# Performance work log

Hardware: AMD Instinct MI355X
Metric: run time of the kernel (lower is better)

## Reference

```python
import jax, jax.numpy as jnp
import numpy as np

NMS_THRESH = 0.5
SCORE_THRESH = 0.05
MAX_DET = 300


def _iou_one_vs_all(box, boxes):
    # box: [4] (x1,y1,x2,y2); boxes: [N,4]
    x1 = jnp.maximum(box[0], boxes[:, 0])
    y1 = jnp.maximum(box[1], boxes[:, 1])
    x2 = jnp.minimum(box[2], boxes[:, 2])
    y2 = jnp.minimum(box[3], boxes[:, 3])
    inter = jnp.maximum(x2 - x1, 0.0) * jnp.maximum(y2 - y1, 0.0)
    area_a = (box[2] - box[0]) * (box[3] - box[1])
    area_b = (boxes[:, 2] - boxes[:, 0]) * (boxes[:, 3] - boxes[:, 1])
    union = area_a + area_b - inter
    return inter / jnp.maximum(union, 1e-8)


def _nms_single_class(boxes, scores):
    # Greedy NMS with max_output_size=MAX_DET, matching tf.image.non_max_suppression
    # after score-threshold prefiltering. boxes:[N,4], scores:[N].
    s0 = jnp.where(scores > SCORE_THRESH, scores, -jnp.inf)

    def step(s, _):
        i = jnp.argmax(s)
        si = s[i]
        sel = jnp.isfinite(si)  # False once no candidates remain
        iou = _iou_one_vs_all(boxes[i], boxes)
        s = jnp.where(sel & (iou > NMS_THRESH), -jnp.inf, s)
        s = s.at[i].set(-jnp.inf)
        return s, (i, si, sel)

    _, (idx, sv, sel) = jax.lax.scan(step, s0, None, length=MAX_DET)
    # unselected slots carry -inf score
    return idx.astype(jnp.int32), jnp.where(sel, sv, -jnp.inf)


def _filter_one_image(boxes, classification, other):
    # boxes:[N,4], classification:[N,C], other:[N,D]
    C = classification.shape[1]
    # class-specific NMS (class_specific_filter=True, nms=True)
    idx, sv = jax.vmap(lambda c: _nms_single_class(boxes, classification[:, c]))(
        jnp.arange(C))  # each [C, MAX_DET]
    labels = jnp.broadcast_to(jnp.arange(C)[:, None], idx.shape)
    cand_scores = sv.reshape(-1)          # [C*MAX_DET]
    cand_idx = idx.reshape(-1)
    cand_lab = labels.reshape(-1)
    # global top-k over all per-class survivors
    top_s, top_i = jax.lax.top_k(cand_scores, MAX_DET)
    sel_idx = cand_idx[top_i]
    sel_lab = cand_lab[top_i]
    valid = jnp.isfinite(top_s)
    # pad invalid slots with -1 (matches tf.pad(..., constant_values=-1))
    out_boxes = jnp.where(valid[:, None], boxes[sel_idx], -1.0)
    out_scores = jnp.where(valid, top_s, -1.0)
    out_labels = jnp.where(valid, sel_lab, -1).astype(jnp.int32)
    out_other = jnp.where(valid[:, None], other[sel_idx], -1.0)
    return out_boxes, out_scores, out_labels, out_other


def setup_inputs() -> dict:
    key = jax.random.key(0)
    k1, k2, k3, k4 = jax.random.split(key, 4)
    B, N, C, D = 16, 50000, 8, 2
    xy = jax.random.uniform(k1, (B, N, 2), jnp.float32, 0.0, 512.0)
    wh = jax.random.uniform(k2, (B, N, 2), jnp.float32, 4.0, 100.0)
    boxes = jnp.concatenate([xy, xy + wh], axis=-1)  # valid (x1,y1,x2,y2)
    classification = jax.random.uniform(k3, (B, N, C), jnp.float32)
    other = jax.random.normal(k4, (B, N, D), jnp.float32)
    return {"boxes": boxes, "classification": classification, "other": other}


def reference(boxes, classification, other):
    # tf.map_fn over batch -> vmap over batch
    return jax.vmap(_filter_one_image)(boxes, classification, other)
```

## Files before the change

kernel.cpp:

```cpp
#include <hip/hip_runtime.h>
#include <math.h>
#include <stdint.h>

#define NB 16
#define NN 50000
#define NC 8
#define ND 2
#define MAX_DET 300
#define NMS_T 0.5f
#define SCORE_T 0.05f
#define CAP 1024
#define CUTBIN 252
#define LBUF 128
#define NTILE32 32
#define CHUNK 256
#define NT 1024
#define NPI (NN * NC)
#define F4PB (NPI / 4 / NTILE32)

typedef unsigned long long u64;

__device__ __forceinline__ float neg_inf() { return -__builtin_inff(); }

__device__ __forceinline__ bool iou_gt(float ax1, float ay1, float ax2, float ay2,
                                       float area_a,
                                       float bx1, float by1, float bx2, float by2,
                                       float area_b) {
    float x1 = fmaxf(ax1, bx1), y1 = fmaxf(ay1, by1);
    float x2 = fminf(ax2, bx2), y2 = fminf(ay2, by2);
    float inter = __fmul_rn(fmaxf(__fsub_rn(x2, x1), 0.0f),
                            fmaxf(__fsub_rn(y2, y1), 0.0f));
    float uni = __fsub_rn(__fadd_rn(area_a, area_b), inter);
    return inter > __fmul_rn(0.5f, fmaxf(uni, 1e-8f));
}

__device__ __forceinline__ u64 score_key(float s, int n) {
    unsigned u = __float_as_uint(s);
    u ^= (u & 0x80000000u) ? 0xFFFFFFFFu : 0x80000000u;
    return ((u64)u << 32) | (unsigned)(~(unsigned)n);
}

__device__ __forceinline__ u64 shfl_xor_u64(u64 v, int m) {
    unsigned lo = (unsigned)v, hi = (unsigned)(v >> 32);
    lo = __shfl_xor(lo, m, 64);
    hi = __shfl_xor(hi, m, 64);
    return ((u64)hi << 32) | lo;
}

__global__ __launch_bounds__(1024) void compact_kernel(
    const float* __restrict__ cls, int* __restrict__ tcnt_g,
    u64* __restrict__ cand)
{
    const int b = blockIdx.x >> 5, t32 = blockIdx.x & 31;
    const int tid = threadIdx.x;
    __shared__ u64 buf[8][LBUF];
    __shared__ int lcnt[8];
    if (tid < 8) lcnt[tid] = 0;
    __syncthreads();

    const float4* c4 = (const float4*)(cls + (size_t)b * NPI);
    const int f0 = t32 * F4PB, fend = f0 + F4PB;

    for (int f = f0 + tid; f < fend; f += 1024) {
        float4 v = c4[f];
        int cb = (f & 1) * 4;
        int n = f >> 1;
        float vv[4] = {v.x, v.y, v.z, v.w};
        #pragma unroll
        for (int k = 0; k < 4; ++k) {
            float s = vv[k];
            if (s > SCORE_T) {
                int bn = (int)(s * 256.0f); if (bn > 255) bn = 255;
                if (bn >= CUTBIN) {
                    int c = cb + k;
                    int pos = atomicAdd(&lcnt[c], 1);
                    if (pos < LBUF) buf[c][pos] = score_key(s, n);
                }
            }
        }
    }
    __syncthreads();
    {
        int c = tid >> 7, i = tid & (LBUF - 1);
        int m = lcnt[c];
        if (i < (m < LBUF ? m : LBUF))
            cand[(size_t)(((b * 8 + c) * NTILE32) + t32) * LBUF + i] = buf[c][i];
        if (i == 0) tcnt_g[(b * 8 + c) * NTILE32 + t32] = m;
    }
}

__global__ __launch_bounds__(NT) void nms_fused(
    const float* __restrict__ boxes, const float* __restrict__ cls,
    const u64* __restrict__ cand, const int* __restrict__ tcnt_g,
    int* __restrict__ sel_idx, float* __restrict__ sel_score)
{
    const int bc = blockIdx.x;
    const int b = bc >> 3, c = bc & 7;
    const int tid = threadIdx.x;
    const int lane = tid & 63;
    const float4* bx4 = (const float4*)(boxes + (size_t)b * NN * 4);
    const float* sr = cls + (size_t)b * NN * NC + c;
    int* si = sel_idx + bc * MAX_DET;
    float* ss = sel_score + bc * MAX_DET;

    __shared__ u64 keys[CAP];
    __shared__ int tcnt_s[NTILE32], toff_s[NTILE32];
    __shared__ int sh_total, sh_ovf;
    __shared__ u64 M64[4][CHUNK];
    __shared__ unsigned presup4[4][CHUNK];
    __shared__ float4 cbox2[2][CHUNK];
    __shared__ float  carea2[2][CHUNK];
    __shared__ int    cidx2[2][CHUNK];
    __shared__ float  cscore2[2][CHUNK];
    __shared__ u64 accs4_s[4];
    __shared__ float4 abox[MAX_DET];
    __shared__ float aarea[MAX_DET];
    __shared__ unsigned bm[(NN + 31) / 32];
    __shared__ float rv[NT];
    __shared__ int   ri[NT];
    __shared__ float sboxsh[5];

    if (tid < 64) {
        int v = (lane < NTILE32) ? tcnt_g[bc * NTILE32 + lane] : 0;
        int incl = v;
        #pragma unroll
        for (int d = 1; d < 32; d <<= 1) {
            int o = __shfl_up(incl, d, 64);
            if (lane >= d) incl += o;
        }
        if (lane < NTILE32) { tcnt_s[lane] = v; toff_s[lane] = incl - v; }
        u64 ov = __ballot(lane < NTILE32 && v > LBUF);
        if (lane == 31) { sh_total = incl; sh_ovf = (ov != 0); }
    }
    __syncthreads();
    const int cnt = sh_total;
    const bool full_fb = sh_ovf || (cnt > CAP);
    const int inSet = cnt < CAP ? cnt : CAP;

    int n_acc = 0;
    if (!full_fb) {
        for (int i = tid; i < CAP; i += NT) keys[i] = 0ull;
        __syncthreads();
        for (int s = tid; s < NTILE32 * LBUF; s += NT) {
            int t = s >> 7, i = s & (LBUF - 1);
            if (i < tcnt_s[t])
                keys[toff_s[t] + i] = cand[(size_t)(bc * NTILE32 + t) * LBUF + i];
        }
        __syncthreads();

        const int p0 = (tid >> 6) * 128 + lane, p1 = p0 + 64;
        u64 v0 = 0, v1 = 0;
        if (tid < 512) {
            v0 = keys[p0]; v1 = keys[p1];
            #pragma unroll
            for (int k = 2; k <= 128; k <<= 1) {
                #pragma unroll
                for (int j = k >> 1; j > 0; j >>= 1) {
                    if (j == 64) {
                        bool dir = ((p0 & k) == 0);
                        if ((v0 < v1) == dir) { u64 t = v0; v0 = v1; v1 = t; }
                    } else {
                        bool lower = ((lane & j) == 0);
                        bool dir0 = ((p0 & k) == 0);
                        bool dir1 = ((p1 & k) == 0);
                        u64 o0 = shfl_xor_u64(v0, j);
                        u64 mx0 = v0 > o0 ? v0 : o0, mn0 = v0 > o0 ? o0 : v0;
                        v0 = (lower == dir0) ? mx0 : mn0;
                        u64 o1 = shfl_xor_u64(v1, j);
                        u64 mx1 = v1 > o1 ? v1 : o1, mn1 = v1 > o1 ? o1 : v1;
                        v1 = (lower == dir1) ? mx1 : mn1;
                    }
                }
            }
        }
        __syncthreads();
        for (int k = 256; k <= CAP; k <<= 1) {
            if (tid < 512) { keys[p0] = v0; keys[p1] = v1; }
            __syncthreads();
            for (int j = k >> 1; j >= 128; j >>= 1) {
                if (tid < 512) {
                    int p = tid;
                    int i = 2 * p - (p & (j - 1));
                    int ix = i + j;
                    bool dir = ((i & k) == 0);
                    u64 a = keys[i], b2 = keys[ix];
                    if ((a < b2) == dir) { keys[i] = b2; keys[ix] = a; }
                }
                __syncthreads();
            }
            if (tid < 512) {
                v0 = keys[p0]; v1 = keys[p1];
                {
                    bool dir = ((p0 & k) == 0);
                    if ((v0 < v1) == dir) { u64 t = v0; v0 = v1; v1 = t; }
                }
                #pragma unroll
                for (int j = 32; j > 0; j >>= 1) {
                    bool lower = ((lane & j) == 0);
                    bool dir = ((p0 & k) == 0);
                    u64 o0 = shfl_xor_u64(v0, j);
                    u64 mx0 = v0 > o0 ? v0 : o0, mn0 = v0 > o0 ? o0 : v0;
                    v0 = (lower == dir) ? mx0 : mn0;
                    u64 o1 = shfl_xor_u64(v1, j);
                    u64 mx1 = v1 > o1 ? v1 : o1, mn1 = v1 > o1 ? o1 : v1;
                    v1 = (lower == dir) ? mx1 : mn1;
                }
            }
            __syncthreads();
        }
        if (tid < 512) { keys[p0] = v0; keys[p1] = v1; }
        __syncthreads();

        if (tid < CHUNK && tid < inSet) {
            u64 key = keys[tid];
            int idx = (int)(~(unsigned)key);
            unsigned u = (unsigned)(key >> 32);
            unsigned uo = (u & 0x80000000u) ? (u ^ 0x80000000u) : (~u);
            float4 bb = bx4[idx];
            cbox2[0][tid] = bb;
            carea2[0][tid] = __fmul_rn(__fsub_rn(bb.z, bb.x), __fsub_rn(bb.w, bb.y));
            cidx2[0][tid] = idx; cscore2[0][tid] = __uint_as_float(uo);
        }
        __syncthreads();

        int base = 0, cur = 0;
        while (n_acc < MAX_DET && base < inSet) {
            int m = inSet - base; if (m > CHUNK) m = CHUNK;

            {
                int i = tid & (CHUNK - 1);
                int q = tid >> 8;
                if (i < m) {
                    float4 B = cbox2[cur][i];
                    float  Barea = carea2[cur][i];
                    unsigned p = 0;
                    int t = q;
                    for (; t + 28 < n_acc; t += 32) {
                        float4 A0 = abox[t];      float r0 = aarea[t];
                        float4 A1 = abox[t + 4];  float r1 = aarea[t + 4];
                        float4 A2 = abox[t + 8];  float r2 = aarea[t + 8];
                        float4 A3 = abox[t + 12]; float r3 = aarea[t + 12];
                        float4 A4 = abox[t + 16]; float r4 = aarea[t + 16];
                        float4 A5 = abox[t + 20]; float r5 = aarea[t + 20];
                        float4 A6 = abox[t + 24]; float r6 = aarea[t + 24];
                        float4 A7 = abox[t + 28]; float r7 = aarea[t + 28];
                        bool s0 = iou_gt(A0.x,A0.y,A0.z,A0.w,r0,B.x,B.y,B.z,B.w,Barea);
                        bool s1 = iou_gt(A1.x,A1.y,A1.z,A1.w,r1,B.x,B.y,B.z,B.w,Barea);
                        bool s2 = iou_gt(A2.x,A2.y,A2.z,A2.w,r2,B.x,B.y,B.z,B.w,Barea);
                        bool s3 = iou_gt(A3.x,A3.y,A3.z,A3.w,r3,B.x,B.y,B.z,B.w,Barea);
                        bool s4 = iou_gt(A4.x,A4.y,A4.z,A4.w,r4,B.x,B.y,B.z,B.w,Barea);
                        bool s5 = iou_gt(A5.x,A5.y,A5.z,A5.w,r5,B.x,B.y,B.z,B.w,Barea);
                        bool s6 = iou_gt(A6.x,A6.y,A6.z,A6.w,r6,B.x,B.y,B.z,B.w,Barea);
                        bool s7 = iou_gt(A7.x,A7.y,A7.z,A7.w,r7,B.x,B.y,B.z,B.w,Barea);
                        if (s0|s1|s2|s3|s4|s5|s6|s7) { p = 1; break; }
                    }
                    if (!p) {
                        for (; t < n_acc; t += 4) {
                            float4 A = abox[t];
                            if (iou_gt(A.x,A.y,A.z,A.w,aarea[t],
                                       B.x,B.y,B.z,B.w,Barea)) { p = 1; break; }
                        }
                    }
                    presup4[q][i] = p;
                    u64 bits = 0;
                    int j0 = q * 64;
                    int jend = i - j0; if (jend > 64) jend = 64; if (jend < 0) jend = 0;
                    int jj = 0;
                    for (; jj + 7 < jend; jj += 8) {
                        int j = j0 + jj;
                        float4 A0 = cbox2[cur][j];     float r0 = carea2[cur][j];
                        float4 A1 = cbox2[cur][j + 1]; float r1 = carea2[cur][j + 1];
                        float4 A2 = cbox2[cur][j + 2]; float r2 = carea2[cur][j + 2];
                        float4 A3 = cbox2[cur][j + 3]; float r3 = carea2[cur][j + 3];
                        float4 A4 = cbox2[cur][j + 4]; float r4 = carea2[cur][j + 4];
                        float4 A5 = cbox2[cur][j + 5]; float r5 = carea2[cur][j + 5];
                        float4 A6 = cbox2[cur][j + 6]; float r6 = carea2[cur][j + 6];
                        float4 A7 = cbox2[cur][j + 7]; float r7 = carea2[cur][j + 7];
                        if (iou_gt(A0.x,A0.y,A0.z,A0.w,r0,B.x,B.y,B.z,B.w,Barea)) bits |= 1ull << jj;
                        if (iou_gt(A1.x,A1.y,A1.z,A1.w,r1,B.x,B.y,B.z,B.w,Barea)) bits |= 1ull << (jj+1);
                        if (iou_gt(A2.x,A2.y,A2.z,A2.w,r2,B.x,B.y,B.z,B.w,Barea)) bits |= 1ull << (jj+2);
                        if (iou_gt(A3.x,A3.y,A3.z,A3.w,r3,B.x,B.y,B.z,B.w,Barea)) bits |= 1ull << (jj+3);
                        if (iou_gt(A4.x,A4.y,A4.z,A4.w,r4,B.x,B.y,B.z,B.w,Barea)) bits |= 1ull << (jj+4);
                        if (iou_gt(A5.x,A5.y,A5.z,A5.w,r5,B.x,B.y,B.z,B.w,Barea)) bits |= 1ull << (jj+5);
                        if (iou_gt(A6.x,A6.y,A6.z,A6.w,r6,B.x,B.y,B.z,B.w,Barea)) bits |= 1ull << (jj+6);
                        if (iou_gt(A7.x,A7.y,A7.z,A7.w,r7,B.x,B.y,B.z,B.w,Barea)) bits |= 1ull << (jj+7);
                    }
                    for (; jj < jend; ++jj) {
                        int j = j0 + jj;
                        float4 A = cbox2[cur][j];
                        if (iou_gt(A.x,A.y,A.z,A.w,carea2[cur][j],
                                   B.x,B.y,B.z,B.w,Barea)) bits |= 1ull << jj;
                    }
                    M64[q][i] = bits;
                }
            }
            __syncthreads();

            int nbase = base + m;
            if (tid < 64) {
                u64 Mr[4][4];
                unsigned pe[4];
                bool acc[4];
                #pragma unroll
                for (int cg = 0; cg < 4; ++cg) {
                    int i = cg * 64 + lane;
                    if (i < m) {
                        pe[cg] = presup4[0][i] | presup4[1][i] | presup4[2][i] | presup4[3][i];
                        #pragma unroll
                        for (int w = 0; w < 4; ++w) Mr[cg][w] = M64[w][i];
                    } else {
                        pe[cg] = 1u;
                        #pragma unroll
                        for (int w = 0; w < 4; ++w) Mr[cg][w] = 0ull;
                    }
                    acc[cg] = (pe[cg] == 0);
                }
                u64 a0 = __ballot(acc[0]), a1 = __ballot(acc[1]);
                u64 a2 = __ballot(acc[2]), a3 = __ballot(acc[3]);
                for (int it = 0; it < CHUNK + 1; ++it) {
                    #pragma unroll
                    for (int cg = 0; cg < 4; ++cg) {
                        u64 sup = (Mr[cg][0] & a0) | (Mr[cg][1] & a1)
                                | (Mr[cg][2] & a2) | (Mr[cg][3] & a3);
                        acc[cg] = (pe[cg] == 0) && (sup == 0ull);
                    }
                    u64 n0 = __ballot(acc[0]), n1 = __ballot(acc[1]);
                    u64 n2 = __ballot(acc[2]), n3 = __ballot(acc[3]);
                    bool same = (n0 == a0) && (n1 == a1) && (n2 == a2) && (n3 == a3);
                    a0 = n0; a1 = n1; a2 = n2; a3 = n3;
                    if (same) break;
                }
                if (lane == 0) { accs4_s[0] = a0; accs4_s[1] = a1;
                                 accs4_s[2] = a2; accs4_s[3] = a3; }
            } else if (tid >= 256 && tid < 512 && nbase < inSet) {
                int w = tid - 256;
                if (nbase + w < inSet) {
                    u64 key = keys[nbase + w];
                    int idx = (int)(~(unsigned)key);
                    unsigned u = (unsigned)(key >> 32);
                    unsigned uo = (u & 0x80000000u) ? (u ^ 0x80000000u) : (~u);
                    float4 bb = bx4[idx];
                    cbox2[cur ^ 1][w] = bb;
                    carea2[cur ^ 1][w] = __fmul_rn(__fsub_rn(bb.z, bb.x), __fsub_rn(bb.w, bb.y));
                    cidx2[cur ^ 1][w] = idx; cscore2[cur ^ 1][w] = __uint_as_float(uo);
                }
            }
            __syncthreads();

            u64 a0 = accs4_s[0], a1 = accs4_s[1], a2 = accs4_s[2], a3 = accs4_s[3];
            int add = __popcll(a0) + __popcll(a1) + __popcll(a2) + __popcll(a3);
            if (tid < m) {
                int gg = tid >> 6, o = tid & 63;
                u64 aw = (gg == 0) ? a0 : (gg == 1) ? a1 : (gg == 2) ? a2 : a3;
                if ((aw >> o) & 1ull) {
                    int rank = 0;
                    if (gg > 0) rank += __popcll(a0);
                    if (gg > 1) rank += __popcll(a1);
                    if (gg > 2) rank += __popcll(a2);
                    rank += __popcll(aw & ((1ull << o) - 1ull));
                    int pos = n_acc + rank;
                    if (pos < MAX_DET) {
                        abox[pos] = cbox2[cur][tid]; aarea[pos] = carea2[cur][tid];
                        si[pos] = cidx2[cur][tid]; ss[pos] = cscore2[cur][tid];
                    }
                }
            }
            n_acc += add; if (n_acc > MAX_DET) n_acc = MAX_DET;
            base = nbase; cur ^= 1;
            __syncthreads();
        }
    }

    const bool part_fb = (!full_fb) && (n_acc < MAX_DET);

    if (full_fb || part_fb) {
        const int BMW = (NN + 31) / 32;
        for (int i = tid; i < BMW; i += NT) bm[i] = 0u;
        __syncthreads();
        if (full_fb) {
            n_acc = 0;
        } else {
            for (int n = tid; n < NN; n += NT) {
                float4 bbn = bx4[n];
                float nb_area = __fmul_rn(__fsub_rn(bbn.z, bbn.x), __fsub_rn(bbn.w, bbn.y));
                int s = 0;
                for (int t = 0; t < n_acc; ++t) {
                    float4 A = abox[t];
                    if (iou_gt(A.x, A.y, A.z, A.w, aarea[t],
                               bbn.x, bbn.y, bbn.z, bbn.w, nb_area)) s = 1;
                }
                if (s) atomicOr(&bm[n >> 5], 1u << (n & 31));
            }
        }
        __syncthreads();

        for (int k = n_acc; k < MAX_DET; ++k) {
            float bv = neg_inf(); int bi = 0x7fffffff;
            for (int n = tid; n < NN; n += NT) {
                if (!((bm[n >> 5] >> (n & 31)) & 1u)) {
                    float v = sr[(size_t)n * NC];
                    if (v > SCORE_T && v > bv) { bv = v; bi = n; }
                }
            }
            rv[tid] = bv; ri[tid] = bi;
            __syncthreads();
            for (int s = NT / 2; s > 0; s >>= 1) {
                if (tid < s) {
                    float ov = rv[tid + s]; int oi = ri[tid + s];
                    if (ov > rv[tid] || (ov == rv[tid] && oi < ri[tid])) { rv[tid] = ov; ri[tid] = oi; }
                }
                __syncthreads();
            }
            float mval = rv[0]; int midx = ri[0];
            if (mval == neg_inf()) {
                for (int kk = k + tid; kk < MAX_DET; kk += NT) { si[kk] = 0; ss[kk] = neg_inf(); }
                break;
            }
            if (tid == 0) {
                si[k] = midx; ss[k] = mval;
                float4 sb = bx4[midx];
                sboxsh[0] = sb.x; sboxsh[1] = sb.y; sboxsh[2] = sb.z; sboxsh[3] = sb.w;
                sboxsh[4] = __fmul_rn(__fsub_rn(sb.z, sb.x), __fsub_rn(sb.w, sb.y));
            }
            __syncthreads();
            float ax1 = sboxsh[0], ay1 = sboxsh[1], ax2 = sboxsh[2], ay2 = sboxsh[3];
            float area_a = sboxsh[4];
            for (int n = tid; n < NN; n += NT) {
                float4 bbn = bx4[n];
                float nb_area = __fmul_rn(__fsub_rn(bbn.z, bbn.x), __fsub_rn(bbn.w, bbn.y));
                if (iou_gt(ax1, ay1, ax2, ay2, area_a,
                           bbn.x, bbn.y, bbn.z, bbn.w, nb_area))
                    atomicOr(&bm[n >> 5], 1u << (n & 31));
            }
            __syncthreads();
        }
    } else {
        for (int kk = n_acc + tid; kk < MAX_DET; kk += NT) { si[kk] = 0; ss[kk] = neg_inf(); }
    }
}

__global__ __launch_bounds__(1024) void topk_kernel(
    const float* __restrict__ boxes, const float* __restrict__ other,
    const int* __restrict__ sel_idx, const float* __restrict__ sel_score,
    float* __restrict__ out)
{
    const int b = blockIdx.x;
    const int tid = threadIdx.x;
    const int NCAND = NC * MAX_DET;
    __shared__ u64 lists[NC][MAX_DET];

    for (int i = tid; i < NCAND; i += 1024) {
        float v = sel_score[b * NCAND + i];
        unsigned u = __float_as_uint(v);
        u ^= (u & 0x80000000u) ? 0xFFFFFFFFu : 0x80000000u;
        lists[i / MAX_DET][i % MAX_DET] = ((u64)u << 32) | (unsigned)(~(unsigned)i);
    }
    __syncthreads();

    const float4* bx4 = (const float4*)(boxes + (size_t)b * NN * 4);
    const float*  ot  = other + (size_t)b * NN * ND;
    float* ob = out;
    float* os = out + NB * MAX_DET * 4;
    float* ol = os + NB * MAX_DET;
    float* oo = ol + NB * MAX_DET;

    for (int i = tid; i < NCAND; i += 1024) {
        int cown = i / MAX_DET, slot = i - cown * MAX_DET;
        u64 K = lists[cown][slot];
        int rank = slot;
        int pos[NC], len[NC];
        #pragma unroll
        for (int c2 = 0; c2 < NC; ++c2) {
            pos[c2] = 0;
            len[c2] = (c2 == cown) ? 0 : MAX_DET;
        }
        for (int step = 0; step < 10; ++step) {
            #pragma unroll
            for (int c2 = 0; c2 < NC; ++c2) {
                if (len[c2] > 0) {
                    int half = len[c2] >> 1;
                    bool go = lists[c2][pos[c2] + half] > K;
                    pos[c2] = go ? pos[c2] + half + 1 : pos[c2];
                    len[c2] = go ? len[c2] - half - 1 : half;
                }
            }
        }
        #pragma unroll
        for (int c2 = 0; c2 < NC; ++c2) rank += pos[c2];

        if (rank < MAX_DET) {
            unsigned u = (unsigned)(K >> 32);
            unsigned uo = (u & 0x80000000u) ? (u ^ 0x80000000u) : (u ^ 0xFFFFFFFFu);
            float score = __uint_as_float(uo);
            bool valid = isfinite(score);
            float b0=-1.f,b1=-1.f,b2=-1.f,b3=-1.f,scv=-1.f,lab=-1.f,o0=-1.f,o1=-1.f;
            if (valid) {
                int n = sel_idx[b * NCAND + i];
                float4 bb = bx4[n];
                b0 = bb.x; b1 = bb.y; b2 = bb.z; b3 = bb.w;
                scv = score; lab = (float)cown;
                o0 = ot[n * ND + 0]; o1 = ot[n * ND + 1];
            }
            int base = b * MAX_DET + rank;
            ob[base * 4 + 0] = b0; ob[base * 4 + 1] = b1;
            ob[base * 4 + 2] = b2; ob[base * 4 + 3] = b3;
            os[base] = scv; ol[base] = lab;
            oo[base * 2 + 0] = o0; oo[base * 2 + 1] = o1;
        }
    }
}

extern "C" void kernel_launch(void* const* d_in, const int* in_sizes, int n_in,
                              void* d_out, int out_size, void* d_ws, size_t ws_size,
                              hipStream_t stream) {
    const float* boxes = (const float*)d_in[0];
    const float* cls   = (const float*)d_in[1];
    const float* other = (const float*)d_in[2];
    float* out = (float*)d_out;

    int* tcnt_g = (int*)d_ws;
    u64* cand  = (u64*)(tcnt_g + NB * NC * NTILE32);
    int* sel_idx = (int*)(cand + (size_t)NB * NC * NTILE32 * LBUF);
    float* sel_score = (float*)(sel_idx + NB * NC * MAX_DET);

    compact_kernel<<<NB * NTILE32, 1024, 0, stream>>>(cls, tcnt_g, cand);
    nms_fused<<<NB * NC, NT, 0, stream>>>(boxes, cls, cand, tcnt_g,
                                          sel_idx, sel_score);
    topk_kernel<<<NB, 1024, 0, stream>>>(boxes, other, sel_idx, sel_score, out);
}
```

Baseline: 66.06 us.

## Split fused NMS into sort, global IoU-matrix, and resolve kernels

Replaces the single fused per-class NMS kernel with three kernels. One sorts the candidates, one builds a 512x512 suppression bitmask matrix in global memory using four times as many small blocks, and one resolves greedy acceptance with a single-wavefront fixed-point iteration. The goal is to spread the quadratic IoU work over more CUs instead of 128 large blocks processed chunk by chunk. The costs are two extra launches and global round-trips for keys and the matrix. The stage is also capped at 512 sorted candidates, so more results depend on the slow full-scan fallback when fewer than 300 are accepted.

```diff
diff --git a/kernel.cpp b/kernel.cpp
--- a/kernel.cpp
+++ b/kernel.cpp
@@ -13,8 +13,7 @@
 #define CUTBIN 252
 #define LBUF 128
 #define NTILE32 32
-#define CHUNK 256
-#define NT 1024
+#define STG 512
 #define NPI (NN * NC)
 #define F4PB (NPI / 4 / NTILE32)
 
@@ -89,9 +88,168 @@
     }
 }
 
-__global__ __launch_bounds__(NT) void nms_fused(
+__global__ __launch_bounds__(512) void sort_kernel(
+    const u64* __restrict__ cand, const int* __restrict__ tcnt_g,
+    u64* __restrict__ skeys, int* __restrict__ meta)
+{
+    const int bc = blockIdx.x;
+    const int tid = threadIdx.x;
+    const int lane = tid & 63;
+    __shared__ u64 keys[CAP];
+    __shared__ int tcnt_s[NTILE32], toff_s[NTILE32];
+    __shared__ int sh_total, sh_ovf;
+
+    if (tid < 64) {
+        int v = (lane < NTILE32) ? tcnt_g[bc * NTILE32 + lane] : 0;
+        int incl = v;
+        #pragma unroll
+        for (int d = 1; d < 32; d <<= 1) {
+            int o = __shfl_up(incl, d, 64);
+            if (lane >= d) incl += o;
+        }
+        if (lane < NTILE32) { tcnt_s[lane] = v; toff_s[lane] = incl - v; }
+        u64 ov = __ballot(lane < NTILE32 && v > LBUF);
+        if (lane == 31) { sh_total = incl; sh_ovf = (ov != 0); }
+    }
+    __syncthreads();
+    const int cnt = sh_total;
+    const bool full_fb = sh_ovf || (cnt > CAP);
+    if (full_fb) {
+        if (tid == 0) meta[bc] = -1;
+        return;
+    }
+    if (tid == 0) meta[bc] = cnt;
+
+    for (int i = tid; i < CAP; i += 512) keys[i] = 0ull;
+    __syncthreads();
+    for (int s = tid; s < NTILE32 * LBUF; s += 512) {
+        int t = s >> 7, i = s & (LBUF - 1);
+        if (i < tcnt_s[t])
+            keys[toff_s[t] + i] = cand[(size_t)(bc * NTILE32 + t) * LBUF + i];
+    }
+    __syncthreads();
+
+    const int p0 = (tid >> 6) * 128 + lane, p1 = p0 + 64;
+    u64 v0 = keys[p0], v1 = keys[p1];
+    #pragma unroll
+    for (int k = 2; k <= 128; k <<= 1) {
+        #pragma unroll
+        for (int j = k >> 1; j > 0; j >>= 1) {
+            if (j == 64) {
+                bool dir = ((p0 & k) == 0);
+                if ((v0 < v1) == dir) { u64 t = v0; v0 = v1; v1 = t; }
+            } else {
+                bool lower = ((lane & j) == 0);
+                bool dir0 = ((p0 & k) == 0);
+                bool dir1 = ((p1 & k) == 0);
+                u64 o0 = shfl_xor_u64(v0, j);
+                u64 mx0 = v0 > o0 ? v0 : o0, mn0 = v0 > o0 ? o0 : v0;
+                v0 = (lower == dir0) ? mx0 : mn0;
+                u64 o1 = shfl_xor_u64(v1, j);
+                u64 mx1 = v1 > o1 ? v1 : o1, mn1 = v1 > o1 ? o1 : v1;
+                v1 = (lower == dir1) ? mx1 : mn1;
+            }
+        }
+    }
+    __syncthreads();
+    for (int k = 256; k <= CAP; k <<= 1) {
+        keys[p0] = v0; keys[p1] = v1;
+        __syncthreads();
+        for (int j = k >> 1; j >= 128; j >>= 1) {
+            int p = tid;
+            int i = 2 * p - (p & (j - 1));
+            int ix = i + j;
+            bool dir = ((i & k) == 0);
+            u64 a = keys[i], b2 = keys[ix];
+            if ((a < b2) == dir) { keys[i] = b2; keys[ix] = a; }
+            __syncthreads();
+        }
+        v0 = keys[p0]; v1 = keys[p1];
+        {
+            bool dir = ((p0 & k) == 0);
+            if ((v0 < v1) == dir) { u64 t = v0; v0 = v1; v1 = t; }
+        }
+        #pragma unroll
+        for (int j = 32; j > 0; j >>= 1) {
+            bool lower = ((lane & j) == 0);
+            bool dir = ((p0 & k) == 0);
+            u64 o0 = shfl_xor_u64(v0, j);
+            u64 mx0 = v0 > o0 ? v0 : o0, mn0 = v0 > o0 ? o0 : v0;
+            v0 = (lower == dir) ? mx0 : mn0;
+            u64 o1 = shfl_xor_u64(v1, j);
+            u64 mx1 = v1 > o1 ? v1 : o1, mn1 = v1 > o1 ? o1 : v1;
+            v1 = (lower == dir) ? mx1 : mn1;
+        }
+        __syncthreads();
+    }
+    skeys[(size_t)bc * CAP + p0] = v0;
+    skeys[(size_t)bc * CAP + p1] = v1;
+}
+
+__global__ __launch_bounds__(128) void matrix_kernel(
+    const float* __restrict__ boxes, const u64* __restrict__ skeys,
+    const int* __restrict__ meta, u64* __restrict__ Mg)
+{
+    const int bc = blockIdx.x >> 2, q = blockIdx.x & 3;
+    const int b = bc >> 3;
+    const int tid = threadIdx.x;
+    const int mcnt = meta[bc];
+    if (mcnt < 0) return;
+    const int inSet = mcnt < CAP ? mcnt : CAP;
+    const int stage = inSet < STG ? inSet : STG;
+
+    __shared__ float4 sbox[STG];
+    __shared__ float  sarea[STG];
+    const float4* bx4 = (const float4*)(boxes + (size_t)b * NN * 4);
+    const u64* sk = skeys + (size_t)bc * CAP;
+
+    for (int i = tid; i < stage; i += 128) {
+        u64 key = sk[i];
+        int idx = (int)(~(unsigned)key);
+        float4 bb = bx4[idx];
+        sbox[i] = bb;
+        sarea[i] = __fmul_rn(__fsub_rn(bb.z, bb.x), __fsub_rn(bb.w, bb.y));
+    }
+    __syncthreads();
+
+    int r = q + 4 * tid;
+    if (r < stage) {
+        float4 B = sbox[r];
+        float Barea = sarea[r];
+        u64* row = Mg + ((size_t)bc * STG + r) * 8;
+        #pragma unroll
+        for (int h = 0; h < 8; ++h) {
+            u64 bits = 0;
+            int j0 = h * 64;
+            int jlim = r - j0;
+            if (jlim > 64) jlim = 64;
+            int jj = 0;
+            for (; jj + 3 < jlim; jj += 4) {
+                int j = j0 + jj;
+                float4 A0 = sbox[j];     float r0 = sarea[j];
+                float4 A1 = sbox[j + 1]; float r1 = sarea[j + 1];
+                float4 A2 = sbox[j + 2]; float r2 = sarea[j + 2];
+                float4 A3 = sbox[j + 3]; float r3 = sarea[j + 3];
+                if (iou_gt(A0.x,A0.y,A0.z,A0.w,r0,B.x,B.y,B.z,B.w,Barea)) bits |= 1ull << jj;
+                if (iou_gt(A1.x,A1.y,A1.z,A1.w,r1,B.x,B.y,B.z,B.w,Barea)) bits |= 1ull << (jj+1);
+                if (iou_gt(A2.x,A2.y,A2.z,A2.w,r2,B.x,B.y,B.z,B.w,Barea)) bits |= 1ull << (jj+2);
+                if (iou_gt(A3.x,A3.y,A3.z,A3.w,r3,B.x,B.y,B.z,B.w,Barea)) bits |= 1ull << (jj+3);
+            }
+            for (; jj < jlim; ++jj) {
+                int j = j0 + jj;
+                float4 A = sbox[j];
+                if (iou_gt(A.x,A.y,A.z,A.w,sarea[j],B.x,B.y,B.z,B.w,Barea))
+                    bits |= 1ull << jj;
+            }
+            row[h] = bits;
+        }
+    }
+}
+
+__global__ __launch_bounds__(512) void resolve_kernel(
     const float* __restrict__ boxes, const float* __restrict__ cls,
-    const u64* __restrict__ cand, const int* __restrict__ tcnt_g,
+    const u64* __restrict__ skeys, const int* __restrict__ meta,
+    const u64* __restrict__ Mg,
     int* __restrict__ sel_idx, float* __restrict__ sel_score)
 {
     const int bc = blockIdx.x;
@@ -100,287 +258,108 @@
     const int lane = tid & 63;
     const float4* bx4 = (const float4*)(boxes + (size_t)b * NN * 4);
     const float* sr = cls + (size_t)b * NN * NC + c;
+    const u64* sk = skeys + (size_t)bc * CAP;
     int* si = sel_idx + bc * MAX_DET;
     float* ss = sel_score + bc * MAX_DET;
 
-    __shared__ u64 keys[CAP];
-    __shared__ int tcnt_s[NTILE32], toff_s[NTILE32];
-    __shared__ int sh_total, sh_ovf;
-    __shared__ u64 M64[4][CHUNK];
-    __shared__ unsigned presup4[4][CHUNK];
-    __shared__ float4 cbox2[2][CHUNK];
-    __shared__ float  carea2[2][CHUNK];
-    __shared__ int    cidx2[2][CHUNK];
-    __shared__ float  cscore2[2][CHUNK];
-    __shared__ u64 accs4_s[4];
+    __shared__ u64 accs_s[8];
     __shared__ float4 abox[MAX_DET];
     __shared__ float aarea[MAX_DET];
     __shared__ unsigned bm[(NN + 31) / 32];
-    __shared__ float rv[NT];
-    __shared__ int   ri[NT];
+    __shared__ float rv[512];
+    __shared__ int   ri[512];
     __shared__ float sboxsh[5];
 
-    if (tid < 64) {
-        int v = (lane < NTILE32) ? tcnt_g[bc * NTILE32 + lane] : 0;
-        int incl = v;
-        #pragma unroll
-        for (int d = 1; d < 32; d <<= 1) {
-            int o = __shfl_up(incl, d, 64);
-            if (lane >= d) incl += o;
-        }
-        if (lane < NTILE32) { tcnt_s[lane] = v; toff_s[lane] = incl - v; }
-        u64 ov = __ballot(lane < NTILE32 && v > LBUF);
-        if (lane == 31) { sh_total = incl; sh_ovf = (ov != 0); }
-    }
-    __syncthreads();
-    const int cnt = sh_total;
-    const bool full_fb = sh_ovf || (cnt > CAP);
-    const int inSet = cnt < CAP ? cnt : CAP;
+    const int mcnt = meta[bc];
+    const bool full_fb = (mcnt < 0);
+    const int inSet = full_fb ? 0 : (mcnt < CAP ? mcnt : CAP);
+    const int stage = inSet < STG ? inSet : STG;
 
     int n_acc = 0;
     if (!full_fb) {
-        for (int i = tid; i < CAP; i += NT) keys[i] = 0ull;
-        __syncthreads();
-        for (int s = tid; s < NTILE32 * LBUF; s += NT) {
-            int t = s >> 7, i = s & (LBUF - 1);
-            if (i < tcnt_s[t])
-                keys[toff_s[t] + i] = cand[(size_t)(bc * NTILE32 + t) * LBUF + i];
-        }
-        __syncthreads();
-
-        const int p0 = (tid >> 6) * 128 + lane, p1 = p0 + 64;
-        u64 v0 = 0, v1 = 0;
-        if (tid < 512) {
-            v0 = keys[p0]; v1 = keys[p1];
+        if (tid < 64) {
+            u64 Mr[8][8];
+            unsigned pe[8];
+            bool acc[8];
             #pragma unroll
-            for (int k = 2; k <= 128; k <<= 1) {
+            for (int cg = 0; cg < 8; ++cg) {
+                int i = cg * 64 + lane;
+                pe[cg] = (i < stage) ? 0u : 1u;
+                const u64* row = Mg + ((size_t)bc * STG + i) * 8;
                 #pragma unroll
-                for (int j = k >> 1; j > 0; j >>= 1) {
-                    if (j == 64) {
-                        bool dir = ((p0 & k) == 0);
-                        if ((v0 < v1) == dir) { u64 t = v0; v0 = v1; v1 = t; }
-                    } else {
-                        bool lower = ((lane & j) == 0);
-                        bool dir0 = ((p0 & k) == 0);
-                        bool dir1 = ((p1 & k) == 0);
-                        u64 o0 = shfl_xor_u64(v0, j);
-                        u64 mx0 = v0 > o0 ? v0 : o0, mn0 = v0 > o0 ? o0 : v0;
-                        v0 = (lower == dir0) ? mx0 : mn0;
-                        u64 o1 = shfl_xor_u64(v1, j);
-                        u64 mx1 = v1 > o1 ? v1 : o1, mn1 = v1 > o1 ? o1 : v1;
-                        v1 = (lower == dir1) ? mx1 : mn1;
+                for (int w = 0; w < 8; ++w) Mr[cg][w] = row[w];
+                acc[cg] = (pe[cg] == 0);
+            }
+            u64 a[8];
+            #pragma unroll
+            for (int h = 0; h < 8; ++h) a[h] = __ballot(acc[h]);
+            for (int it = 0; it < STG + 8; ++it) {
+                #pragma unroll
+                for (int cg = 0; cg < 8; ++cg) {
+                    u64 sup = 0;
+                    #pragma unroll
+                    for (int h = 0; h < 8; ++h) sup |= Mr[cg][h] & a[h];
+                    acc[cg] = (pe[cg] == 0) && (sup == 0ull);
+                }
+                u64 nb[8]; bool same = true;
+                #pragma unroll
+                for (int h = 0; h < 8; ++h) {
+                    nb[h] = __ballot(acc[h]);
+                    same = same && (nb[h] == a[h]);
+                    a[h] = nb[h];
+                }
+                if (same) break;
+            }
+            if (lane == 0) {
+                #pragma unroll
+                for (int h = 0; h < 8; ++h) accs_s[h] = a[h];
+            }
+        }
+        __syncthreads();
+
+        {
+            u64 a[8]; int tot = 0;
+            #pragma unroll
+            for (int h = 0; h < 8; ++h) { a[h] = accs_s[h]; tot += __popcll(a[h]); }
+            n_acc = tot < MAX_DET ? tot : MAX_DET;
+            if (tid < stage) {
+                int cg = tid >> 6, o = tid & 63;
+                if ((a[cg] >> o) & 1ull) {
+                    int rank = 0;
+                    for (int h = 0; h < cg; ++h) rank += __popcll(a[h]);
+                    rank += __popcll(a[cg] & ((o == 0) ? 0ull : ((1ull << o) - 1ull)));
+                    if (rank < MAX_DET) {
+                        u64 key = sk[tid];
+                        int idx = (int)(~(unsigned)key);
+                        unsigned u = (unsigned)(key >> 32);
+                        unsigned uo = (u & 0x80000000u) ? (u ^ 0x80000000u) : (~u);
+                        si[rank] = idx; ss[rank] = __uint_as_float(uo);
                     }
                 }
             }
         }
         __syncthreads();
-        for (int k = 256; k <= CAP; k <<= 1) {
-            if (tid < 512) { keys[p0] = v0; keys[p1] = v1; }
-            __syncthreads();
-            for (int j = k >> 1; j >= 128; j >>= 1) {
-                if (tid < 512) {
-                    int p = tid;
-                    int i = 2 * p - (p & (j - 1));
-                    int ix = i + j;
-                    bool dir = ((i & k) == 0);
-                    u64 a = keys[i], b2 = keys[ix];
-                    if ((a < b2) == dir) { keys[i] = b2; keys[ix] = a; }
-                }
-                __syncthreads();
-            }
-            if (tid < 512) {
-                v0 = keys[p0]; v1 = keys[p1];
-                {
-                    bool dir = ((p0 & k) == 0);
-                    if ((v0 < v1) == dir) { u64 t = v0; v0 = v1; v1 = t; }
-                }
-                #pragma unroll
-                for (int j = 32; j > 0; j >>= 1) {
-                    bool lower = ((lane & j) == 0);
-                    bool dir = ((p0 & k) == 0);
-                    u64 o0 = shfl_xor_u64(v0, j);
-                    u64 mx0 = v0 > o0 ? v0 : o0, mn0 = v0 > o0 ? o0 : v0;
-                    v0 = (lower == dir) ? mx0 : mn0;
-                    u64 o1 = shfl_xor_u64(v1, j);
-                    u64 mx1 = v1 > o1 ? v1 : o1, mn1 = v1 > o1 ? o1 : v1;
-                    v1 = (lower == dir) ? mx1 : mn1;
-                }
-            }
-            __syncthreads();
-        }
-        if (tid < 512) { keys[p0] = v0; keys[p1] = v1; }
-        __syncthreads();
-
-        if (tid < CHUNK && tid < inSet) {
-            u64 key = keys[tid];
-            int idx = (int)(~(unsigned)key);
-            unsigned u = (unsigned)(key >> 32);
-            unsigned uo = (u & 0x80000000u) ? (u ^ 0x80000000u) : (~u);
-            float4 bb = bx4[idx];
-            cbox2[0][tid] = bb;
-            carea2[0][tid] = __fmul_rn(__fsub_rn(bb.z, bb.x), __fsub_rn(bb.w, bb.y));
-            cidx2[0][tid] = idx; cscore2[0][tid] = __uint_as_float(uo);
-        }
-        __syncthreads();
-
-        int base = 0, cur = 0;
-        while (n_acc < MAX_DET && base < inSet) {
-            int m = inSet - base; if (m > CHUNK) m = CHUNK;
-
-            {
-                int i = tid & (CHUNK - 1);
-                int q = tid >> 8;
-                if (i < m) {
-                    float4 B = cbox2[cur][i];
-                    float  Barea = carea2[cur][i];
-                    unsigned p = 0;
-                    int t = q;
-                    for (; t + 28 < n_acc; t += 32) {
-                        float4 A0 = abox[t];      float r0 = aarea[t];
-                        float4 A1 = abox[t + 4];  float r1 = aarea[t + 4];
-                        float4 A2 = abox[t + 8];  float r2 = aarea[t + 8];
-                        float4 A3 = abox[t + 12]; float r3 = aarea[t + 12];
-                        float4 A4 = abox[t + 16]; float r4 = aarea[t + 16];
-                        float4 A5 = abox[t + 20]; float r5 = aarea[t + 20];
-                        float4 A6 = abox[t + 24]; float r6 = aarea[t + 24];
-                        float4 A7 = abox[t + 28]; float r7 = aarea[t + 28];
-                        bool s0 = iou_gt(A0.x,A0.y,A0.z,A0.w,r0,B.x,B.y,B.z,B.w,Barea);
-                        bool s1 = iou_gt(A1.x,A1.y,A1.z,A1.w,r1,B.x,B.y,B.z,B.w,Barea);
-                        bool s2 = iou_gt(A2.x,A2.y,A2.z,A2.w,r2,B.x,B.y,B.z,B.w,Barea);
-                        bool s3 = iou_gt(A3.x,A3.y,A3.z,A3.w,r3,B.x,B.y,B.z,B.w,Barea);
-                        bool s4 = iou_gt(A4.x,A4.y,A4.z,A4.w,r4,B.x,B.y,B.z,B.w,Barea);
-                        bool s5 = iou_gt(A5.x,A5.y,A5.z,A5.w,r5,B.x,B.y,B.z,B.w,Barea);
-                        bool s6 = iou_gt(A6.x,A6.y,A6.z,A6.w,r6,B.x,B.y,B.z,B.w,Barea);
-                        bool s7 = iou_gt(A7.x,A7.y,A7.z,A7.w,r7,B.x,B.y,B.z,B.w,Barea);
-                        if (s0|s1|s2|s3|s4|s5|s6|s7) { p = 1; break; }
-                    }
-                    if (!p) {
-                        for (; t < n_acc; t += 4) {
-                            float4 A = abox[t];
-                            if (iou_gt(A.x,A.y,A.z,A.w,aarea[t],
-                                       B.x,B.y,B.z,B.w,Barea)) { p = 1; break; }
-                        }
-                    }
-                    presup4[q][i] = p;
-                    u64 bits = 0;
-                    int j0 = q * 64;
-                    int jend = i - j0; if (jend > 64) jend = 64; if (jend < 0) jend = 0;
-                    int jj = 0;
-                    for (; jj + 7 < jend; jj += 8) {
-                        int j = j0 + jj;
-                        float4 A0 = cbox2[cur][j];     float r0 = carea2[cur][j];
-                        float4 A1 = cbox2[cur][j + 1]; float r1 = carea2[cur][j + 1];
-                        float4 A2 = cbox2[cur][j + 2]; float r2 = carea2[cur][j + 2];
-                        float4 A3 = cbox2[cur][j + 3]; float r3 = carea2[cur][j + 3];
-                        float4 A4 = cbox2[cur][j + 4]; float r4 = carea2[cur][j + 4];
-                        float4 A5 = cbox2[cur][j + 5]; float r5 = carea2[cur][j + 5];
-                        float4 A6 = cbox2[cur][j + 6]; float r6 = carea2[cur][j + 6];
-                        float4 A7 = cbox2[cur][j + 7]; float r7 = carea2[cur][j + 7];
-                        if (iou_gt(A0.x,A0.y,A0.z,A0.w,r0,B.x,B.y,B.z,B.w,Barea)) bits |= 1ull << jj;
-                        if (iou_gt(A1.x,A1.y,A1.z,A1.w,r1,B.x,B.y,B.z,B.w,Barea)) bits |= 1ull << (jj+1);
-                        if (iou_gt(A2.x,A2.y,A2.z,A2.w,r2,B.x,B.y,B.z,B.w,Barea)) bits |= 1ull << (jj+2);
-                        if (iou_gt(A3.x,A3.y,A3.z,A3.w,r3,B.x,B.y,B.z,B.w,Barea)) bits |= 1ull << (jj+3);
-                        if (iou_gt(A4.x,A4.y,A4.z,A4.w,r4,B.x,B.y,B.z,B.w,Barea)) bits |= 1ull << (jj+4);
-                        if (iou_gt(A5.x,A5.y,A5.z,A5.w,r5,B.x,B.y,B.z,B.w,Barea)) bits |= 1ull << (jj+5);
-                        if (iou_gt(A6.x,A6.y,A6.z,A6.w,r6,B.x,B.y,B.z,B.w,Barea)) bits |= 1ull << (jj+6);
-                        if (iou_gt(A7.x,A7.y,A7.z,A7.w,r7,B.x,B.y,B.z,B.w,Barea)) bits |= 1ull << (jj+7);
-                    }
-                    for (; jj < jend; ++jj) {
-                        int j = j0 + jj;
-                        float4 A = cbox2[cur][j];
-                        if (iou_gt(A.x,A.y,A.z,A.w,carea2[cur][j],
-                                   B.x,B.y,B.z,B.w,Barea)) bits |= 1ull << jj;
-                    }
-                    M64[q][i] = bits;
-                }
-            }
-            __syncthreads();
-
-            int nbase = base + m;
-            if (tid < 64) {
-                u64 Mr[4][4];
-                unsigned pe[4];
-                bool acc[4];
-                #pragma unroll
-                for (int cg = 0; cg < 4; ++cg) {
-                    int i = cg * 64 + lane;
-                    if (i < m) {
-                        pe[cg] = presup4[0][i] | presup4[1][i] | presup4[2][i] | presup4[3][i];
-                        #pragma unroll
-                        for (int w = 0; w < 4; ++w) Mr[cg][w] = M64[w][i];
-                    } else {
-                        pe[cg] = 1u;
-                        #pragma unroll
-                        for (int w = 0; w < 4; ++w) Mr[cg][w] = 0ull;
-                    }
-                    acc[cg] = (pe[cg] == 0);
-                }
-                u64 a0 = __ballot(acc[0]), a1 = __ballot(acc[1]);
-                u64 a2 = __ballot(acc[2]), a3 = __ballot(acc[3]);
-                for (int it = 0; it < CHUNK + 1; ++it) {
-                    #pragma unroll
-                    for (int cg = 0; cg < 4; ++cg) {
-                        u64 sup = (Mr[cg][0] & a0) | (Mr[cg][1] & a1)
-                                | (Mr[cg][2] & a2) | (Mr[cg][3] & a3);
-                        acc[cg] = (pe[cg] == 0) && (sup == 0ull);
-                    }
-                    u64 n0 = __ballot(acc[0]), n1 = __ballot(acc[1]);
-                    u64 n2 = __ballot(acc[2]), n3 = __ballot(acc[3]);
-                    bool same = (n0 == a0) && (n1 == a1) && (n2 == a2) && (n3 == a3);
-                    a0 = n0; a1 = n1; a2 = n2; a3 = n3;
-                    if (same) break;
-                }
-                if (lane == 0) { accs4_s[0] = a0; accs4_s[1] = a1;
-                                 accs4_s[2] = a2; accs4_s[3] = a3; }
-            } else if (tid >= 256 && tid < 512 && nbase < inSet) {
-                int w = tid - 256;
-                if (nbase + w < inSet) {
-                    u64 key = keys[nbase + w];
-                    int idx = (int)(~(unsigned)key);
-                    unsigned u = (unsigned)(key >> 32);
-                    unsigned uo = (u & 0x80000000u) ? (u ^ 0x80000000u) : (~u);
-                    float4 bb = bx4[idx];
-                    cbox2[cur ^ 1][w] = bb;
-                    carea2[cur ^ 1][w] = __fmul_rn(__fsub_rn(bb.z, bb.x), __fsub_rn(bb.w, bb.y));
-                    cidx2[cur ^ 1][w] = idx; cscore2[cur ^ 1][w] = __uint_as_float(uo);
-                }
-            }
-            __syncthreads();
-
-            u64 a0 = accs4_s[0], a1 = accs4_s[1], a2 = accs4_s[2], a3 = accs4_s[3];
-            int add = __popcll(a0) + __popcll(a1) + __popcll(a2) + __popcll(a3);
-            if (tid < m) {
-                int gg = tid >> 6, o = tid & 63;
-                u64 aw = (gg == 0) ? a0 : (gg == 1) ? a1 : (gg == 2) ? a2 : a3;
-                if ((aw >> o) & 1ull) {
-                    int rank = 0;
-                    if (gg > 0) rank += __popcll(a0);
-                    if (gg > 1) rank += __popcll(a1);
-                    if (gg > 2) rank += __popcll(a2);
-                    rank += __popcll(aw & ((1ull << o) - 1ull));
-                    int pos = n_acc + rank;
-                    if (pos < MAX_DET) {
-                        abox[pos] = cbox2[cur][tid]; aarea[pos] = carea2[cur][tid];
-                        si[pos] = cidx2[cur][tid]; ss[pos] = cscore2[cur][tid];
-                    }
-                }
-            }
-            n_acc += add; if (n_acc > MAX_DET) n_acc = MAX_DET;
-            base = nbase; cur ^= 1;
-            __syncthreads();
-        }
     }
 
     const bool part_fb = (!full_fb) && (n_acc < MAX_DET);
 
     if (full_fb || part_fb) {
+        if (part_fb) {
+            for (int t = tid; t < n_acc; t += 512) {
+                int n = si[t];
+                float4 bb = bx4[n];
+                abox[t] = bb;
+                aarea[t] = __fmul_rn(__fsub_rn(bb.z, bb.x), __fsub_rn(bb.w, bb.y));
+            }
+        }
+        __syncthreads();
         const int BMW = (NN + 31) / 32;
-        for (int i = tid; i < BMW; i += NT) bm[i] = 0u;
+        for (int i = tid; i < BMW; i += 512) bm[i] = 0u;
         __syncthreads();
         if (full_fb) {
             n_acc = 0;
         } else {
-            for (int n = tid; n < NN; n += NT) {
+            for (int n = tid; n < NN; n += 512) {
                 float4 bbn = bx4[n];
                 float nb_area = __fmul_rn(__fsub_rn(bbn.z, bbn.x), __fsub_rn(bbn.w, bbn.y));
                 int s = 0;
@@ -396,7 +375,7 @@
 
         for (int k = n_acc; k < MAX_DET; ++k) {
             float bv = neg_inf(); int bi = 0x7fffffff;
-            for (int n = tid; n < NN; n += NT) {
+            for (int n = tid; n < NN; n += 512) {
                 if (!((bm[n >> 5] >> (n & 31)) & 1u)) {
                     float v = sr[(size_t)n * NC];
                     if (v > SCORE_T && v > bv) { bv = v; bi = n; }
@@ -404,7 +383,7 @@
             }
             rv[tid] = bv; ri[tid] = bi;
             __syncthreads();
-            for (int s = NT / 2; s > 0; s >>= 1) {
+            for (int s = 256; s > 0; s >>= 1) {
                 if (tid < s) {
                     float ov = rv[tid + s]; int oi = ri[tid + s];
                     if (ov > rv[tid] || (ov == rv[tid] && oi < ri[tid])) { rv[tid] = ov; ri[tid] = oi; }
@@ -413,7 +392,7 @@
             }
             float mval = rv[0]; int midx = ri[0];
             if (mval == neg_inf()) {
-                for (int kk = k + tid; kk < MAX_DET; kk += NT) { si[kk] = 0; ss[kk] = neg_inf(); }
+                for (int kk = k + tid; kk < MAX_DET; kk += 512) { si[kk] = 0; ss[kk] = neg_inf(); }
                 break;
             }
             if (tid == 0) {
@@ -425,7 +404,7 @@
             __syncthreads();
             float ax1 = sboxsh[0], ay1 = sboxsh[1], ax2 = sboxsh[2], ay2 = sboxsh[3];
             float area_a = sboxsh[4];
-            for (int n = tid; n < NN; n += NT) {
+            for (int n = tid; n < NN; n += 512) {
                 float4 bbn = bx4[n];
                 float nb_area = __fmul_rn(__fsub_rn(bbn.z, bbn.x), __fsub_rn(bbn.w, bbn.y));
                 if (iou_gt(ax1, ay1, ax2, ay2, area_a,
@@ -434,8 +413,6 @@
             }
             __syncthreads();
         }
-    } else {
-        for (int kk = n_acc + tid; kk < MAX_DET; kk += NT) { si[kk] = 0; ss[kk] = neg_inf(); }
     }
 }
 
@@ -519,12 +496,17 @@
     float* out = (float*)d_out;
 
     int* tcnt_g = (int*)d_ws;
-    u64* cand  = (u64*)(tcnt_g + NB * NC * NTILE32);
-    int* sel_idx = (int*)(cand + (size_t)NB * NC * NTILE32 * LBUF);
+    int* meta   = tcnt_g + NB * NC * NTILE32;
+    u64* cand   = (u64*)(meta + 128);
+    u64* skeys  = cand + (size_t)NB * NC * NTILE32 * LBUF;
+    u64* Mg     = skeys + (size_t)NB * NC * CAP;
+    int* sel_idx = (int*)(Mg + (size_t)NB * NC * STG * 8);
     float* sel_score = (float*)(sel_idx + NB * NC * MAX_DET);
 
     compact_kernel<<<NB * NTILE32, 1024, 0, stream>>>(cls, tcnt_g, cand);
-    nms_fused<<<NB * NC, NT, 0, stream>>>(boxes, cls, cand, tcnt_g,
-                                          sel_idx, sel_score);
+    sort_kernel<<<NB * NC, 512, 0, stream>>>(cand, tcnt_g, skeys, meta);
+    matrix_kernel<<<NB * NC * 4, 128, 0, stream>>>(boxes, skeys, meta, Mg);
+    resolve_kernel<<<NB * NC, 512, 0, stream>>>(boxes, cls, skeys, meta, Mg,
+                                                sel_idx, sel_score);
     topk_kernel<<<NB, 1024, 0, stream>>>(boxes, other, sel_idx, sel_score, out);
 }
```

After: 84.08 us. +27.3%, slower.
